# Performance work log

Hardware: AMD Instinct MI355X
Metric: run time of the kernel (lower is better)

The kernel has to match this reference:

```python
import jax, jax.numpy as jnp
import numpy as np

SIZE_DICT = 1024
DIM_DICT = 256
BETA = 0.001


def setup_inputs() -> dict:
    key = jax.random.key(0)
    k1, k2 = jax.random.split(key)
    z = jax.random.normal(k1, (64, 1024, DIM_DICT), dtype=jnp.float32)
    codebook = jax.random.normal(k2, (SIZE_DICT, DIM_DICT), dtype=jnp.float32)
    return {"z": z, "codebook": codebook, "flg_train": 1}


def reference(z, codebook, flg_train):
    zf = z.reshape(-1, DIM_DICT)  # [N, D]
    # squared euclidean distances: ||z||^2 + ||c||^2 - 2 z c^T  -> [N, K]
    d = (jnp.sum(zf ** 2, axis=1, keepdims=True)
         + jnp.sum(codebook ** 2, axis=1)
         - 2.0 * jnp.matmul(zf, codebook.T))
    idx = jnp.argmin(d, axis=1)  # [N]
    # one-hot @ codebook == gather
    z_q = codebook[idx].reshape(z.shape)
    if flg_train:
        loss = (jnp.mean((jax.lax.stop_gradient(z_q) - z) ** 2)
                + BETA * jnp.mean((z_q - jax.lax.stop_gradient(z)) ** 2))
    else:
        loss = jnp.float32(0.0)
    # straight-through estimator
    z_q = z + jax.lax.stop_gradient(z_q - z)
    # perplexity from codebook usage histogram (== mean of one-hot rows)
    n = zf.shape[0]
    counts = jax.ops.segment_sum(jnp.ones((n,), jnp.float32), idx,
                                 num_segments=SIZE_DICT)
    e_mean = counts / n
    perplexity = jnp.exp(-jnp.sum(e_mean * jnp.log(e_mean + 1e-10)))
    return (z_q, loss, perplexity)
```

## Files before the change

kernel.cpp:

```cpp
#include <hip/hip_runtime.h>


#define N_ROWS 65536
#define DIM    256
#define K_CODES 1024
#define BETA   0.001f

#define BM      128
#define NBLOCKS (N_ROWS / BM)
#define NTHREADS 512
#define CHUNK_BYTES 65536
#define NCHUNK  16

#define LO_SCALE 2048.0f
#define LO_INV   (1.0f / 2048.0f)

#define WS_BESTS_OFF 16384
#define WS_CBIMG_OFF 278528
#define WS_NEED (WS_CBIMG_OFF + NCHUNK * CHUNK_BYTES)

typedef _Float16 f16x8 __attribute__((ext_vector_type(8)));
typedef float f32x16 __attribute__((ext_vector_type(16)));


__global__ void cnorm_kernel(const float* __restrict__ cb, float* __restrict__ cnorm) {
    int k = blockIdx.x * blockDim.x + threadIdx.x;
    if (k >= K_CODES) return;
    const float4* row = (const float4*)(cb + (size_t)k * DIM);
    float s = 0.f;
#pragma unroll
    for (int j = 0; j < DIM / 4; ++j) {
        float4 v = row[j];
        s = fmaf(v.x, v.x, s);
        s = fmaf(v.y, v.y, s);
        s = fmaf(v.z, v.z, s);
        s = fmaf(v.w, v.w, s);
    }
    cnorm[k] = s;
}

__global__ void cb_prep(const float* __restrict__ cb, char* __restrict__ img) {
    int idx = blockIdx.x * blockDim.x + threadIdx.x;
    int c   = idx >> 5;
    int g32 = idx & 31;
    const float4* src = (const float4*)(cb + (size_t)c * DIM + g32 * 8);
    float4 v0 = src[0], v1 = src[1];
    float vv[8] = {v0.x, v0.y, v0.z, v0.w, v1.x, v1.y, v1.z, v1.w};
    f16x8 hi, lo;
#pragma unroll
    for (int j = 0; j < 8; ++j) {
        _Float16 h = (_Float16)vv[j];
        hi[j] = h;
        lo[j] = (_Float16)((vv[j] - (float)h) * LO_SCALE);
    }
    int kh = g32 >> 4;
    int gl = g32 & 15;
    int cl = c & 63;
    int gp = gl ^ (cl & 7);
    int unit = (c >> 6) * 2 + kh;
    size_t off = (size_t)unit * 32768 + (size_t)cl * 256 + (size_t)gp * 16;
    *(f16x8*)(img + off) = hi;
    *(f16x8*)(img + off + 16384) = lo;
}


__device__ inline void stage_chunk(const char* img, int c, char* ldsbase, int tid) {
#pragma unroll
    for (int i = 0; i < 8; ++i) {
        __builtin_amdgcn_global_load_lds(
            (const __attribute__((address_space(1))) unsigned int*)
                (img + (size_t)c * CHUNK_BYTES + i * 8192 + tid * 16),
            (__attribute__((address_space(3))) unsigned int*)
                (ldsbase + i * 8192 + tid * 16),
            16, 0, 0);
    }
}

#define COMPUTE_HALF(KH, BUF)                                                        \
    {                                                                                \
        const _Float16* ch_row = csb + (BUF) * 32768 + (KH) * 16384 + crow * 128;    \
        const _Float16* cl_row = ch_row + 8192;                                      \
        _Pragma("unroll")                                                            \
        for (int ks = 0; ks < 8; ++ks) {                                             \
            int gb = (ks * 2 + lh) ^ csw;                                            \
            f16x8 bh = *(const f16x8*)(ch_row + gb * 8);                             \
            f16x8 bl = *(const f16x8*)(cl_row + gb * 8);                             \
            f16x8 ah = zh[(KH) * 8 + ks];                                            \
            f16x8 al = zl[(KH) * 8 + ks];                                            \
            acc_hh = __builtin_amdgcn_mfma_f32_32x32x16_f16(ah, bh, acc_hh, 0, 0, 0);\
            acc_x  = __builtin_amdgcn_mfma_f32_32x32x16_f16(ah, bl, acc_x, 0, 0, 0); \
            acc_x  = __builtin_amdgcn_mfma_f32_32x32x16_f16(al, bh, acc_x, 0, 0, 0); \
        }                                                                            \
    }

__global__ __launch_bounds__(NTHREADS, 2)
void vq_main_mfma(const float* __restrict__ z, const char* __restrict__ img,
                  const float* __restrict__ cnorm, int* __restrict__ bests_g,
                  int* __restrict__ counts, float* __restrict__ ploss) {
    __shared__ _Float16 csb[2 * 32768];
    __shared__ float bs2[BM][2];
    __shared__ int   bc2[BM][2];
    __shared__ float znorm_lds[BM];
    __shared__ float red[NTHREADS];

    const int tid  = threadIdx.x;
    const int lane = tid & 63;
    const int w    = tid >> 6;
    const int wr   = w >> 1;
    const int wc   = w & 1;
    const int l31  = lane & 31;
    const int lh   = lane >> 5;
    const int r0   = blockIdx.x * BM;

    stage_chunk(img, 0, (char*)csb, tid);

    const int zrow = wr * 32 + l31;
    f16x8 zh[16], zl[16];
    {
        const float* zr = z + (size_t)(r0 + zrow) * DIM;
        float zn = 0.f;
#pragma unroll
        for (int gi = 0; gi < 16; ++gi) {
            int g = gi * 2 + lh;
            float4 v0 = *(const float4*)(zr + g * 8);
            float4 v1 = *(const float4*)(zr + g * 8 + 4);
            float vv[8] = {v0.x, v0.y, v0.z, v0.w, v1.x, v1.y, v1.z, v1.w};
            f16x8 hi, lo;
#pragma unroll
            for (int j = 0; j < 8; ++j) {
                _Float16 h = (_Float16)vv[j];
                hi[j] = h;
                lo[j] = (_Float16)((vv[j] - (float)h) * LO_SCALE);
                zn = fmaf(vv[j], vv[j], zn);
            }
            zh[gi] = hi;
            zl[gi] = lo;
        }
        zn += __shfl_xor(zn, 32, 64);
        if (wc == 0 && lh == 0) znorm_lds[zrow] = zn;
    }

    f32x16 acc_hh, acc_x;
#pragma unroll
    for (int e = 0; e < 16; ++e) { acc_hh[e] = 0.f; acc_x[e] = 0.f; }
    float best_s[16];
    int   best_c[16];
#pragma unroll
    for (int e = 0; e < 16; ++e) { best_s[e] = 3.4e38f; best_c[e] = 0; }

    const int crow = wc * 32 + l31;
    const int csw  = crow & 7;

#pragma unroll 1
    for (int c = 0; c < NCHUNK; ++c) {
        const int b = c & 1;
        asm volatile("" ::: "memory");
        __builtin_amdgcn_s_barrier();
        asm volatile("" ::: "memory");
        if (c + 1 < NCHUNK) {
            stage_chunk(img, c + 1, (char*)csb + (b ^ 1) * CHUNK_BYTES, tid);
            asm volatile("s_waitcnt vmcnt(8)" ::: "memory");
        } else {
            asm volatile("s_waitcnt vmcnt(0)" ::: "memory");
        }
        __builtin_amdgcn_s_barrier();
        asm volatile("" ::: "memory");

        __builtin_amdgcn_s_setprio(1);
        COMPUTE_HALF(0, b)
        COMPUTE_HALF(1, b)
        __builtin_amdgcn_s_setprio(0);

        {
            int col = c * 64 + crow;
            float cn = cnorm[col];
#pragma unroll
            for (int rg = 0; rg < 16; ++rg) {
                float s = fmaf(-2.0f, fmaf(acc_x[rg], LO_INV, acc_hh[rg]), cn);
                bool take = s < best_s[rg];
                best_s[rg] = take ? s : best_s[rg];
                best_c[rg] = take ? col : best_c[rg];
            }
#pragma unroll
            for (int e = 0; e < 16; ++e) { acc_hh[e] = 0.f; acc_x[e] = 0.f; }
        }
    }

#pragma unroll
    for (int rg = 0; rg < 16; ++rg) {
        float bsv = best_s[rg];
        int   bcv = best_c[rg];
#pragma unroll
        for (int s = 1; s < 32; s <<= 1) {
            float os = __shfl_xor(bsv, s, 64);
            int   oc = __shfl_xor(bcv, s, 64);
            bool take = (os < bsv) || (os == bsv && oc < bcv);
            bsv = take ? os : bsv;
            bcv = take ? oc : bcv;
        }
        best_s[rg] = bsv;
        best_c[rg] = bcv;
    }
    if (l31 == 0) {
#pragma unroll
        for (int rg = 0; rg < 16; ++rg) {
            int rl = (rg & 3) + 8 * (rg >> 2) + 4 * lh;
            bs2[wr * 32 + rl][wc] = best_s[rg];
            bc2[wr * 32 + rl][wc] = best_c[rg];
        }
    }
    __syncthreads();

    float lsum = 0.f;
    if (tid < BM) {
        float s0 = bs2[tid][0], s1 = bs2[tid][1];
        int   c0 = bc2[tid][0], c1 = bc2[tid][1];
        bool t1 = (s1 < s0) || (s1 == s0 && c1 < c0);
        int   bc = t1 ? c1 : c0;
        float bs = t1 ? s1 : s0;
        bests_g[r0 + tid] = bc;
        atomicAdd(&counts[bc], 1);
        lsum = bs + znorm_lds[tid];
    }
    red[tid] = lsum;
    __syncthreads();
    for (int s = NTHREADS / 2; s > 0; s >>= 1) {
        if (tid < s) red[tid] += red[tid + s];
        __syncthreads();
    }
    if (tid == 0) ploss[blockIdx.x] = red[0];
}


__global__ __launch_bounds__(256)
void vq_gather(const float4* __restrict__ cb4, const int* __restrict__ bests,
               float4* __restrict__ out4) {
    int gid = blockIdx.x * blockDim.x + threadIdx.x;
    int row = gid >> 6;
    int q   = gid & 63;
    out4[gid] = cb4[(size_t)bests[row] * 64 + q];
}


#define FBM     32
#define FCHUNK  512
#define FDSTAGE 16
#define FCS_PAD 20
#define FNBLOCKS (N_ROWS / FBM)

__global__ __launch_bounds__(256, 2)
void vq_main_fp32(const float* __restrict__ z, const float* __restrict__ cb,
                  const float* __restrict__ cnorm, float* __restrict__ out,
                  int* __restrict__ counts, float* __restrict__ ploss) {
    __shared__ float zs[FBM][DIM];
    __shared__ float cs[FCHUNK][FCS_PAD];
    __shared__ int   bests[FBM];
    __shared__ float red[256];

    const int tid = threadIdx.x;
    const int tx  = tid & 63;
    const int ty  = tid >> 6;
    const int r0  = blockIdx.x * FBM;

    {
        const float4* zg  = (const float4*)(z + (size_t)r0 * DIM);
        float4*       zsv = (float4*)&zs[0][0];
#pragma unroll
        for (int j = 0; j < (FBM * DIM / 4) / 256; ++j)
            zsv[tid + 256 * j] = zg[tid + 256 * j];
    }

    unsigned long long best[8];
#pragma unroll
    for (int i = 0; i < 8; ++i) best[i] = ~0ull;

    for (int cb0 = 0; cb0 < K_CODES; cb0 += FCHUNK) {
        float acc[8][8];
#pragma unroll
        for (int i = 0; i < 8; ++i)
#pragma unroll
            for (int m = 0; m < 8; ++m) acc[i][m] = 0.f;

        for (int sd = 0; sd < DIM / FDSTAGE; ++sd) {
            __syncthreads();
#pragma unroll
            for (int j = 0; j < 8; ++j) {
                int f4i = tid + 256 * j;
                int c   = f4i >> 2;
                int qq  = f4i & 3;
                float4 v = *(const float4*)(cb + (size_t)(cb0 + c) * DIM + sd * FDSTAGE + qq * 4);
                *(float4*)&cs[c][qq * 4] = v;
            }
            __syncthreads();

#pragma unroll
            for (int dd4 = 0; dd4 < FDSTAGE / 4; ++dd4) {
                float4 zv[8], cv[8];
#pragma unroll
                for (int i = 0; i < 8; ++i)
                    zv[i] = *(const float4*)&zs[ty * 8 + i][sd * FDSTAGE + dd4 * 4];
#pragma unroll
                for (int m = 0; m < 8; ++m)
                    cv[m] = *(const float4*)&cs[tx + 64 * m][dd4 * 4];
#pragma unroll
                for (int i = 0; i < 8; ++i)
#pragma unroll
                    for (int m = 0; m < 8; ++m) {
                        float a = acc[i][m];
                        a = fmaf(zv[i].x, cv[m].x, a);
                        a = fmaf(zv[i].y, cv[m].y, a);
                        a = fmaf(zv[i].z, cv[m].z, a);
                        a = fmaf(zv[i].w, cv[m].w, a);
                        acc[i][m] = a;
                    }
            }
        }

#pragma unroll
        for (int m = 0; m < 8; ++m) {
            int   c  = cb0 + tx + 64 * m;
            float cn = cnorm[c];
#pragma unroll
            for (int i = 0; i < 8; ++i) {
                float s = fmaf(-2.f, acc[i][m], cn);
                unsigned u = __float_as_uint(s);
                u = (u & 0x80000000u) ? ~u : (u | 0x80000000u);
                unsigned long long key = ((unsigned long long)u << 32) | (unsigned)c;
                best[i] = key < best[i] ? key : best[i];
            }
        }
    }

#pragma unroll
    for (int i = 0; i < 8; ++i) {
        unsigned long long b = best[i];
#pragma unroll
        for (int s = 1; s < 64; s <<= 1) {
            unsigned long long o = __shfl_xor(b, s, 64);
            b = o < b ? o : b;
        }
        best[i] = b;
    }
    if (tx == 0)
#pragma unroll
        for (int i = 0; i < 8; ++i)
            bests[ty * 8 + i] = (int)(best[i] & 0xFFFFFFFFu);
    __syncthreads();

    const int r  = tid >> 3;
    const int lq = tid & 7;
    const int bidx = bests[r];
    const float4* crow = (const float4*)(cb + (size_t)bidx * DIM);
    const float4* zrow = (const float4*)&zs[r][0];
    float4*       orow = (float4*)(out + (size_t)(r0 + r) * DIM);
    float lsum = 0.f;
#pragma unroll
    for (int j = 0; j < 8; ++j) {
        int qg = lq + j * 8;
        float4 c4 = crow[qg];
        float4 z4 = zrow[qg];
        float4 o;
        float dx = c4.x - z4.x; o.x = z4.x + dx; lsum = fmaf(dx, dx, lsum);
        float dy = c4.y - z4.y; o.y = z4.y + dy; lsum = fmaf(dy, dy, lsum);
        float dz = c4.z - z4.z; o.z = z4.z + dz; lsum = fmaf(dz, dz, lsum);
        float dw = c4.w - z4.w; o.w = z4.w + dw; lsum = fmaf(dw, dw, lsum);
        orow[qg] = o;
    }
    if (tid < FBM) atomicAdd(&counts[bests[tid]], 1);

    red[tid] = lsum;
    __syncthreads();
    for (int s = 128; s > 0; s >>= 1) {
        if (tid < s) red[tid] += red[tid + s];
        __syncthreads();
    }
    if (tid == 0) ploss[blockIdx.x] = red[0];
}


__global__ void vq_final(const float* __restrict__ ploss, const int* __restrict__ counts,
                         const int* __restrict__ flg, float* __restrict__ out2, int np) {
    __shared__ float red[1024];
    const int t = threadIdx.x;

    float l = 0.f;
    for (int i = t; i < np; i += 1024) l += ploss[i];
    red[t] = l;
    __syncthreads();
    for (int s = 512; s > 0; s >>= 1) {
        if (t < s) red[t] += red[t + s];
        __syncthreads();
    }
    if (t == 0) {
        float loss = (red[0] / (float)((size_t)N_ROWS * DIM)) * (1.0f + BETA);
        if (flg[0] == 0) loss = 0.f;
        out2[0] = loss;
    }
    __syncthreads();

    float e = (float)counts[t] / (float)N_ROWS;
    red[t] = e * logf(e + 1e-10f);
    __syncthreads();
    for (int s = 512; s > 0; s >>= 1) {
        if (t < s) red[t] += red[t + s];
        __syncthreads();
    }
    if (t == 0) out2[1] = expf(-red[0]);
}

extern "C" void kernel_launch(void* const* d_in, const int* in_sizes, int n_in,
                              void* d_out, int out_size, void* d_ws, size_t ws_size,
                              hipStream_t stream) {
    const float* z   = (const float*)d_in[0];
    const float* cb  = (const float*)d_in[1];
    const int*   flg = (const int*)d_in[2];
    float* out = (float*)d_out;
    float* ws  = (float*)d_ws;

    float* cnorm  = ws;
    int*   counts = (int*)((char*)d_ws + 4096);
    float* ploss  = (float*)((char*)d_ws + 8192);
    int*   bests  = (int*)((char*)d_ws + WS_BESTS_OFF);
    char*  cbimg  = (char*)d_ws + WS_CBIMG_OFF;

    hipMemsetAsync(counts, 0, K_CODES * sizeof(int), stream);
    cnorm_kernel<<<K_CODES / 256, 256, 0, stream>>>(cb, cnorm);

    if (ws_size >= (size_t)WS_NEED) {
        cb_prep<<<128, 256, 0, stream>>>(cb, cbimg);
        vq_main_mfma<<<NBLOCKS, NTHREADS, 0, stream>>>(z, cbimg, cnorm, bests, counts, ploss);
        vq_gather<<<(N_ROWS * 64) / 256, 256, 0, stream>>>((const float4*)cb, bests, (float4*)out);
        vq_final<<<1, 1024, 0, stream>>>(ploss, counts, flg, out + (size_t)N_ROWS * DIM, NBLOCKS);
    } else {
        vq_main_fp32<<<FNBLOCKS, 256, 0, stream>>>(z, cb, cnorm, out, counts, ploss);
        vq_final<<<1, 1024, 0, stream>>>(ploss, counts, flg, out + (size_t)N_ROWS * DIM, FNBLOCKS);
    }
}
```

Before: 176.5 us.

## Halve block tile to 64 rows and stream codebook in half-K units

Shrinks each block to 64 rows and 256 threads, and splits each 64-code chunk into two 32KB K-half units that are double-buffered in LDS. This halves LDS use per block and doubles the block count, aiming for more resident blocks and finer-grained overlap of staging with MFMA work. In exchange, the codebook is re-read from L2 twice as often per row, the loop runs twice as many barriers, and the z register fragments are now indexed by a runtime K-half. That runtime index may push those fragments to scratch or add selects.

```diff
diff --git a/kernel.cpp b/kernel.cpp
--- a/kernel.cpp
+++ b/kernel.cpp
@@ -6,18 +6,18 @@
 #define K_CODES 1024
 #define BETA   0.001f
 
-#define BM      128
+#define BM      64
 #define NBLOCKS (N_ROWS / BM)
-#define NTHREADS 512
-#define CHUNK_BYTES 65536
-#define NCHUNK  16
+#define NTHREADS 256
+#define UNIT_BYTES 32768
+#define NUNIT   32
 
 #define LO_SCALE 2048.0f
 #define LO_INV   (1.0f / 2048.0f)
 
 #define WS_BESTS_OFF 16384
 #define WS_CBIMG_OFF 278528
-#define WS_NEED (WS_CBIMG_OFF + NCHUNK * CHUNK_BYTES)
+#define WS_NEED (WS_CBIMG_OFF + NUNIT * UNIT_BYTES)
 
 typedef _Float16 f16x8 __attribute__((ext_vector_type(8)));
 typedef float f32x16 __attribute__((ext_vector_type(16)));
@@ -58,46 +58,29 @@
     int cl = c & 63;
     int gp = gl ^ (cl & 7);
     int unit = (c >> 6) * 2 + kh;
-    size_t off = (size_t)unit * 32768 + (size_t)cl * 256 + (size_t)gp * 16;
+    size_t off = (size_t)unit * UNIT_BYTES + (size_t)cl * 256 + (size_t)gp * 16;
     *(f16x8*)(img + off) = hi;
     *(f16x8*)(img + off + 16384) = lo;
 }
 
 
-__device__ inline void stage_chunk(const char* img, int c, char* ldsbase, int tid) {
+__device__ inline void stage_unit(const char* img, int u, char* ldsbase, int tid) {
 #pragma unroll
     for (int i = 0; i < 8; ++i) {
         __builtin_amdgcn_global_load_lds(
             (const __attribute__((address_space(1))) unsigned int*)
-                (img + (size_t)c * CHUNK_BYTES + i * 8192 + tid * 16),
+                (img + (size_t)u * UNIT_BYTES + i * 4096 + tid * 16),
             (__attribute__((address_space(3))) unsigned int*)
-                (ldsbase + i * 8192 + tid * 16),
+                (ldsbase + i * 4096 + tid * 16),
             16, 0, 0);
     }
 }
-
-#define COMPUTE_HALF(KH, BUF)                                                        \
-    {                                                                                \
-        const _Float16* ch_row = csb + (BUF) * 32768 + (KH) * 16384 + crow * 128;    \
-        const _Float16* cl_row = ch_row + 8192;                                      \
-        _Pragma("unroll")                                                            \
-        for (int ks = 0; ks < 8; ++ks) {                                             \
-            int gb = (ks * 2 + lh) ^ csw;                                            \
-            f16x8 bh = *(const f16x8*)(ch_row + gb * 8);                             \
-            f16x8 bl = *(const f16x8*)(cl_row + gb * 8);                             \
-            f16x8 ah = zh[(KH) * 8 + ks];                                            \
-            f16x8 al = zl[(KH) * 8 + ks];                                            \
-            acc_hh = __builtin_amdgcn_mfma_f32_32x32x16_f16(ah, bh, acc_hh, 0, 0, 0);\
-            acc_x  = __builtin_amdgcn_mfma_f32_32x32x16_f16(ah, bl, acc_x, 0, 0, 0); \
-            acc_x  = __builtin_amdgcn_mfma_f32_32x32x16_f16(al, bh, acc_x, 0, 0, 0); \
-        }                                                                            \
-    }
 
 __global__ __launch_bounds__(NTHREADS, 2)
 void vq_main_mfma(const float* __restrict__ z, const char* __restrict__ img,
                   const float* __restrict__ cnorm, int* __restrict__ bests_g,
                   int* __restrict__ counts, float* __restrict__ ploss) {
-    __shared__ _Float16 csb[2 * 32768];
+    __shared__ _Float16 csb[2 * 16384];
     __shared__ float bs2[BM][2];
     __shared__ int   bc2[BM][2];
     __shared__ float znorm_lds[BM];
@@ -112,7 +95,7 @@
     const int lh   = lane >> 5;
     const int r0   = blockIdx.x * BM;
 
-    stage_chunk(img, 0, (char*)csb, tid);
+    stage_unit(img, 0, (char*)csb, tid);
 
     const int zrow = wr * 32 + l31;
     f16x8 zh[16], zl[16];
@@ -152,13 +135,13 @@
     const int csw  = crow & 7;
 
 #pragma unroll 1
-    for (int c = 0; c < NCHUNK; ++c) {
-        const int b = c & 1;
+    for (int u = 0; u < NUNIT; ++u) {
+        const int b = u & 1;
         asm volatile("" ::: "memory");
         __builtin_amdgcn_s_barrier();
         asm volatile("" ::: "memory");
-        if (c + 1 < NCHUNK) {
-            stage_chunk(img, c + 1, (char*)csb + (b ^ 1) * CHUNK_BYTES, tid);
+        if (u + 1 < NUNIT) {
+            stage_unit(img, u + 1, (char*)csb + (b ^ 1) * UNIT_BYTES, tid);
             asm volatile("s_waitcnt vmcnt(8)" ::: "memory");
         } else {
             asm volatile("s_waitcnt vmcnt(0)" ::: "memory");
@@ -166,13 +149,26 @@
         __builtin_amdgcn_s_barrier();
         asm volatile("" ::: "memory");
 
+        const int kh = u & 1;
+        const _Float16* ch_row = csb + b * 16384 + crow * 128;
+        const _Float16* cl_row = ch_row + 8192;
+
         __builtin_amdgcn_s_setprio(1);
-        COMPUTE_HALF(0, b)
-        COMPUTE_HALF(1, b)
+#pragma unroll
+        for (int ks = 0; ks < 8; ++ks) {
+            int gb = (ks * 2 + lh) ^ csw;
+            f16x8 bh = *(const f16x8*)(ch_row + gb * 8);
+            f16x8 bl = *(const f16x8*)(cl_row + gb * 8);
+            f16x8 ah = zh[kh * 8 + ks];
+            f16x8 al = zl[kh * 8 + ks];
+            acc_hh = __builtin_amdgcn_mfma_f32_32x32x16_f16(ah, bh, acc_hh, 0, 0, 0);
+            acc_x  = __builtin_amdgcn_mfma_f32_32x32x16_f16(ah, bl, acc_x, 0, 0, 0);
+            acc_x  = __builtin_amdgcn_mfma_f32_32x32x16_f16(al, bh, acc_x, 0, 0, 0);
+        }
         __builtin_amdgcn_s_setprio(0);
 
-        {
-            int col = c * 64 + crow;
+        if (kh == 1) {
+            int col = (u >> 1) * 64 + crow;
             float cn = cnorm[col];
 #pragma unroll
             for (int rg = 0; rg < 16; ++rg) {
```

Result: slower. 395.3 us (+124.0%).

## Transpose codebook LDS image to group-major layout and split cross accumulator

Applied to the files above, without the earlier changes.

Changes the prepped codebook image from a row-major, XOR-swizzled layout to a group-major layout in which consecutive codes are contiguous for each 8-element k-group, so lanes read consecutive 16-byte words from LDS without a swizzle. The cross-term accumulator is split into two independent accumulators so that back-to-back MFMAs no longer depend on the same destination, and the two are summed before the distance update. This is meant to cut LDS bank conflicts and MFMA dependency stalls, at the cost of 16 more accumulator registers per thread, which may pressure occupancy at launch bounds of 2.

```diff
diff --git a/kernel.cpp b/kernel.cpp
--- a/kernel.cpp
+++ b/kernel.cpp
@@ -56,9 +56,8 @@
     int kh = g32 >> 4;
     int gl = g32 & 15;
     int cl = c & 63;
-    int gp = gl ^ (cl & 7);
     int unit = (c >> 6) * 2 + kh;
-    size_t off = (size_t)unit * 32768 + (size_t)cl * 256 + (size_t)gp * 16;
+    size_t off = (size_t)unit * 32768 + (size_t)gl * 1024 + (size_t)cl * 16;
     *(f16x8*)(img + off) = hi;
     *(f16x8*)(img + off + 16384) = lo;
 }
@@ -76,20 +75,18 @@
     }
 }
 
-#define COMPUTE_HALF(KH, BUF)                                                        \
+#define COMPUTE_CHUNK(BUF)                                                           \
     {                                                                                \
-        const _Float16* ch_row = csb + (BUF) * 32768 + (KH) * 16384 + crow * 128;    \
-        const _Float16* cl_row = ch_row + 8192;                                      \
+        const _Float16* bbase = csb + (BUF) * 32768 + crow * 8;                      \
         _Pragma("unroll")                                                            \
-        for (int ks = 0; ks < 8; ++ks) {                                             \
-            int gb = (ks * 2 + lh) ^ csw;                                            \
-            f16x8 bh = *(const f16x8*)(ch_row + gb * 8);                             \
-            f16x8 bl = *(const f16x8*)(cl_row + gb * 8);                             \
-            f16x8 ah = zh[(KH) * 8 + ks];                                            \
-            f16x8 al = zl[(KH) * 8 + ks];                                            \
+        for (int ks = 0; ks < 16; ++ks) {                                            \
+            const _Float16* p = bbase + (ks >> 3) * 16384 + ((ks & 7) * 2 + lh) * 512;\
+            f16x8 bh = *(const f16x8*)(p);                                           \
+            f16x8 bl = *(const f16x8*)(p + 8192);                                    \
+            f16x8 ah = zh[ks], al = zl[ks];                                          \
             acc_hh = __builtin_amdgcn_mfma_f32_32x32x16_f16(ah, bh, acc_hh, 0, 0, 0);\
-            acc_x  = __builtin_amdgcn_mfma_f32_32x32x16_f16(ah, bl, acc_x, 0, 0, 0); \
-            acc_x  = __builtin_amdgcn_mfma_f32_32x32x16_f16(al, bh, acc_x, 0, 0, 0); \
+            acc_x1 = __builtin_amdgcn_mfma_f32_32x32x16_f16(ah, bl, acc_x1, 0, 0, 0);\
+            acc_x2 = __builtin_amdgcn_mfma_f32_32x32x16_f16(al, bh, acc_x2, 0, 0, 0);\
         }                                                                            \
     }
 
@@ -140,16 +137,15 @@
         if (wc == 0 && lh == 0) znorm_lds[zrow] = zn;
     }
 
-    f32x16 acc_hh, acc_x;
-#pragma unroll
-    for (int e = 0; e < 16; ++e) { acc_hh[e] = 0.f; acc_x[e] = 0.f; }
+    f32x16 acc_hh, acc_x1, acc_x2;
+#pragma unroll
+    for (int e = 0; e < 16; ++e) { acc_hh[e] = 0.f; acc_x1[e] = 0.f; acc_x2[e] = 0.f; }
     float best_s[16];
     int   best_c[16];
 #pragma unroll
     for (int e = 0; e < 16; ++e) { best_s[e] = 3.4e38f; best_c[e] = 0; }
 
     const int crow = wc * 32 + l31;
-    const int csw  = crow & 7;
 
 #pragma unroll 1
     for (int c = 0; c < NCHUNK; ++c) {
@@ -167,8 +163,7 @@
         asm volatile("" ::: "memory");
 
         __builtin_amdgcn_s_setprio(1);
-        COMPUTE_HALF(0, b)
-        COMPUTE_HALF(1, b)
+        COMPUTE_CHUNK(b)
         __builtin_amdgcn_s_setprio(0);
 
         {
@@ -176,13 +171,14 @@
             float cn = cnorm[col];
 #pragma unroll
             for (int rg = 0; rg < 16; ++rg) {
-                float s = fmaf(-2.0f, fmaf(acc_x[rg], LO_INV, acc_hh[rg]), cn);
+                float dot = fmaf(acc_x1[rg] + acc_x2[rg], LO_INV, acc_hh[rg]);
+                float s = fmaf(-2.0f, dot, cn);
                 bool take = s < best_s[rg];
                 best_s[rg] = take ? s : best_s[rg];
                 best_c[rg] = take ? col : best_c[rg];
             }
 #pragma unroll
-            for (int e = 0; e < 16; ++e) { acc_hh[e] = 0.f; acc_x[e] = 0.f; }
+            for (int e = 0; e < 16; ++e) { acc_hh[e] = 0.f; acc_x1[e] = 0.f; acc_x2[e] = 0.f; }
         }
     }
 
```

Result: no change. 175.2 us (-0.7%).
